# Kernel tuning notes

Hardware: AMD Instinct MI355X
Metric: run time of the kernel (lower is better)

The kernel has to match this reference:

```python
import jax, jax.numpy as jnp
import numpy as np

B, H, S, D = 4, 16, 2048, 64


def setup_inputs() -> dict:
    key = jax.random.key(0)
    kq, kk, kv = jax.random.split(key, 3)
    q = jax.random.normal(kq, (B, H, S, D), dtype=jnp.float32)
    k = jax.random.normal(kk, (B, H, S, D), dtype=jnp.float32)
    v = jax.random.normal(kv, (B, H, S, D), dtype=jnp.float32)
    # causal mask: 1 = keep, 0 = masked (matches masked_fill(mask == 0, -10000))
    mask = jnp.tril(jnp.ones((S, S), dtype=jnp.int32))[None, None, :, :]
    return {"q": q, "k": k, "v": v, "mask": mask}


def reference(q, k, v, mask):
    head_dim = q.shape[3]
    # [b,h,s,t] attention logits
    attn = jnp.einsum("bhsd,bhtd->bhst", q, k) / jnp.sqrt(jnp.float32(head_dim))
    attn = jnp.where(mask == 0, jnp.float32(-10000.0), attn)
    score = jax.nn.softmax(attn, axis=-1)
    # dropout is identity at inference (eval mode)
    return jnp.einsum("bhst,bhtd->bhsd", score, v)
```

## Files before the change

kernel.cpp:

```cpp
#include <hip/hip_runtime.h>
#include <hip/hip_bf16.h>

typedef __bf16 bf16_t;
typedef bf16_t bf16x8 __attribute__((ext_vector_type(8)));
typedef float  f32x4  __attribute__((ext_vector_type(4)));
typedef float  f32x16 __attribute__((ext_vector_type(16)));
typedef int    i32x4  __attribute__((ext_vector_type(4)));

#define DH 64

__device__ __forceinline__ unsigned pkbf(float a, float b) {
    union { bf16_t h[2]; unsigned u; } z;
    z.h[0] = (bf16_t)a; z.h[1] = (bf16_t)b;
    return z.u;
}


__global__ __launch_bounds__(256, 2)
void sdpa_fwd(const float* __restrict__ Qg, const float* __restrict__ Kg,
              const float* __restrict__ Vg, float* __restrict__ Og)
{
    __shared__ char lds[2 * 16384];

    const int n  = blockIdx.x;
    const int o  = ((n & 7) << 6) | (n >> 3);
    const int bh = o >> 3;
    const int pr = o & 7;

    const int t   = threadIdx.x;
    const int w   = t >> 6;
    const int l31 = t & 31;
    const int hi  = (t >> 5) & 1;
    const int swk = (l31 & 7) << 4;

    const size_t hoff = (size_t)bh * 2048 * DH;
    const float* Qh = Qg + hoff;
    const float* Kh = Kg + hoff;
    const float* Vh = Vg + hoff;
    float*       Oh = Og + hoff;

    const int srow = (t >> 3) * 2;
    const int sdc  = t & 7;

    f32x4 rk[4], rv[4];
    {
        const float* kp = Kh + (size_t)srow * DH + sdc * 8;
        rk[0] = *(const f32x4*)kp;        rk[1] = *(const f32x4*)(kp + 4);
        rk[2] = *(const f32x4*)(kp + DH); rk[3] = *(const f32x4*)(kp + DH + 4);
        const float* vp = Vh + (size_t)srow * DH + sdc * 8;
        rv[0] = *(const f32x4*)vp;        rv[1] = *(const f32x4*)(vp + 4);
        rv[2] = *(const f32x4*)(vp + DH); rv[3] = *(const f32x4*)(vp + DH + 4);
    }

    const int stripes[2] = { 15 - pr, pr };
    int gt = 0;

    for (int s = 0; s < 2; ++s) {
        const int p    = stripes[s];
        const int qS   = p * 128;
        const int nkt  = 2 * p + 2;
        const int qsb  = qS + w * 32;
        const int qrow = qsb + l31;
        const int ktd  = qsb >> 6;

        bf16x8 qf[4];
#pragma unroll
        for (int sd = 0; sd < 4; ++sd) {
            const float* qp = Qh + (size_t)qrow * DH + sd * 16 + hi * 8;
            f32x4 a = *(const f32x4*)qp;
            f32x4 b = *(const f32x4*)(qp + 4);
            bf16x8 f;
            f[0] = (bf16_t)(a[0]*0.125f); f[1] = (bf16_t)(a[1]*0.125f);
            f[2] = (bf16_t)(a[2]*0.125f); f[3] = (bf16_t)(a[3]*0.125f);
            f[4] = (bf16_t)(b[0]*0.125f); f[5] = (bf16_t)(b[1]*0.125f);
            f[6] = (bf16_t)(b[2]*0.125f); f[7] = (bf16_t)(b[3]*0.125f);
            qf[sd] = f;
        }

        f32x16 acc0 = {}, acc1 = {};
        float m_run = -1e30f, l_run = 0.0f;

        for (int kt = 0; kt < nkt; ++kt, ++gt) {
            char* kb_ = lds + (gt & 1) * 16384;
            char* vb_ = kb_ + 8192;

            {
#pragma unroll
                for (int r2 = 0; r2 < 2; ++r2) {
                    const int key = srow + r2;
                    bf16x8 f;
                    f[0] = (bf16_t)rk[r2*2][0]; f[1] = (bf16_t)rk[r2*2][1];
                    f[2] = (bf16_t)rk[r2*2][2]; f[3] = (bf16_t)rk[r2*2][3];
                    f[4] = (bf16_t)rk[r2*2+1][0]; f[5] = (bf16_t)rk[r2*2+1][1];
                    f[6] = (bf16_t)rk[r2*2+1][2]; f[7] = (bf16_t)rk[r2*2+1][3];
                    *(bf16x8*)(kb_ + ((key * 128 + sdc * 16) ^ ((key & 7) << 4))) = f;
                }
#pragma unroll
                for (int jj = 0; jj < 8; ++jj) {
                    const int d  = sdc * 8 + jj;
                    const float x0 = (jj < 4) ? rv[0][jj & 3] : rv[1][jj & 3];
                    const float x1 = (jj < 4) ? rv[2][jj & 3] : rv[3][jj & 3];
                    *(unsigned*)(vb_ + ((d * 128 + srow * 2) ^ (((jj ^ sdc) & 7) << 4)))
                        = pkbf(x0, x1);
                }
            }
            if (!(s == 1 && kt == nkt - 1)) {
                const int nk = (kt + 1 < nkt) ? kt + 1 : 0;
                const float* kp = Kh + (size_t)(nk * 64 + srow) * DH + sdc * 8;
                rk[0] = *(const f32x4*)kp;        rk[1] = *(const f32x4*)(kp + 4);
                rk[2] = *(const f32x4*)(kp + DH); rk[3] = *(const f32x4*)(kp + DH + 4);
                const float* vp = Vh + (size_t)(nk * 64 + srow) * DH + sdc * 8;
                rv[0] = *(const f32x4*)vp;        rv[1] = *(const f32x4*)(vp + 4);
                rv[2] = *(const f32x4*)(vp + DH); rv[3] = *(const f32x4*)(vp + DH + 4);
            }
            __syncthreads();

            if (kt * 64 <= qsb + 31) {
                f32x16 tf0 = {}, tf1 = {};
#pragma unroll
                for (int sd = 0; sd < 4; ++sd) {
                    const int inner = sd * 32 + hi * 16;
                    const bf16x8 k0 = *(const bf16x8*)(kb_ + ((l31 * 128 + inner) ^ swk));
                    const bf16x8 k1 = *(const bf16x8*)(kb_ + (((32 + l31) * 128 + inner) ^ swk));
                    tf0 = __builtin_amdgcn_mfma_f32_32x32x16_bf16(k0, qf[sd], tf0, 0, 0, 0);
                    tf1 = __builtin_amdgcn_mfma_f32_32x32x16_bf16(k1, qf[sd], tf1, 0, 0, 0);
                }

                if (kt == ktd) {
#pragma unroll
                    for (int r = 0; r < 16; ++r) {
                        const int krow = kt * 64 + (r & 3) + 8 * (r >> 2) + 4 * hi;
                        if (krow > qrow)      tf0[r] = -10000.0f;
                        if (krow + 32 > qrow) tf1[r] = -10000.0f;
                    }
                }

                float mx = tf0[0];
#pragma unroll
                for (int r = 1; r < 16; ++r) mx = fmaxf(mx, tf0[r]);
#pragma unroll
                for (int r = 0; r < 16; ++r) mx = fmaxf(mx, tf1[r]);
                mx = fmaxf(mx, __shfl_xor(mx, 32));

                if (!__all(mx <= m_run + 8.0f)) {
                    const float mnew  = fmaxf(m_run, mx);
                    const float alpha = __expf(m_run - mnew);
                    m_run = mnew;
                    l_run *= alpha;
                    acc0 *= alpha;
                    acc1 *= alpha;
                }

                float sum = 0.0f;
#pragma unroll
                for (int r = 0; r < 16; ++r) { tf0[r] = __expf(tf0[r] - m_run); sum += tf0[r]; }
#pragma unroll
                for (int r = 0; r < 16; ++r) { tf1[r] = __expf(tf1[r] - m_run); sum += tf1[r]; }
                sum += __shfl_xor(sum, 32);
                l_run += sum;

                unsigned P0[2][4], P1[2][4];
#pragma unroll
                for (int rg = 0; rg < 4; ++rg) {
                    P0[0][rg] = pkbf(tf0[rg * 4 + 0], tf0[rg * 4 + 1]);
                    P1[0][rg] = pkbf(tf0[rg * 4 + 2], tf0[rg * 4 + 3]);
                    P0[1][rg] = pkbf(tf1[rg * 4 + 0], tf1[rg * 4 + 1]);
                    P1[1][rg] = pkbf(tf1[rg * 4 + 2], tf1[rg * 4 + 3]);
                }

#pragma unroll
                for (int sidx = 0; sidx < 4; ++sidx) {
                    const int kb  = sidx >> 1;
                    const int rgl = (sidx & 1) * 2, rgh = rgl + 1;
                    int w0, w1, w2, w3;
#if defined(__has_builtin) && __has_builtin(__builtin_amdgcn_permlane32_swap)
                    auto r0 = __builtin_amdgcn_permlane32_swap((int)P0[kb][rgl], (int)P0[kb][rgh], false, false);
                    auto r1 = __builtin_amdgcn_permlane32_swap((int)P1[kb][rgl], (int)P1[kb][rgh], false, false);
                    w0 = r0[0]; w2 = r0[1]; w1 = r1[0]; w3 = r1[1];
#else
                    const int sa0 = __shfl_xor((int)P0[kb][rgl], 32);
                    const int sb0 = __shfl_xor((int)P0[kb][rgh], 32);
                    const int sa1 = __shfl_xor((int)P1[kb][rgl], 32);
                    const int sb1 = __shfl_xor((int)P1[kb][rgh], 32);
                    w0 = hi ? sb0 : (int)P0[kb][rgl];
                    w2 = hi ? (int)P0[kb][rgh] : sa0;
                    w1 = hi ? sb1 : (int)P1[kb][rgl];
                    w3 = hi ? (int)P1[kb][rgh] : sa1;
#endif
                    union { i32x4 i; bf16x8 v; } pz;
                    pz.i = (i32x4){ w0, w1, w2, w3 };

                    const int inner = sidx * 32 + hi * 16;
                    const int d0 = l31;
                    const int d1 = 32 + l31;
                    const int sz0 = (((d0 & 7) ^ (d0 >> 3)) & 7) << 4;
                    const int sz1 = (((d1 & 7) ^ (d1 >> 3)) & 7) << 4;
                    const bf16x8 v0 = *(const bf16x8*)(vb_ + ((d0 * 128 + inner) ^ sz0));
                    const bf16x8 v1 = *(const bf16x8*)(vb_ + ((d1 * 128 + inner) ^ sz1));
                    acc0 = __builtin_amdgcn_mfma_f32_32x32x16_bf16(v0, pz.v, acc0, 0, 0, 0);
                    acc1 = __builtin_amdgcn_mfma_f32_32x32x16_bf16(v1, pz.v, acc1, 0, 0, 0);
                }
            }
        }

        const float inv = 1.0f / l_run;
        float* op = Oh + (size_t)qrow * DH;
#pragma unroll
        for (int rq = 0; rq < 4; ++rq) {
            f32x4 o0, o1;
#pragma unroll
            for (int j = 0; j < 4; ++j) {
                o0[j] = acc0[rq * 4 + j] * inv;
                o1[j] = acc1[rq * 4 + j] * inv;
            }
            *(f32x4*)(op + 8 * rq + 4 * hi)      = o0;
            *(f32x4*)(op + 32 + 8 * rq + 4 * hi) = o1;
        }
    }
}

extern "C" void kernel_launch(void* const* d_in, const int* in_sizes, int n_in,
                              void* d_out, int out_size, void* d_ws, size_t ws_size,
                              hipStream_t stream) {
    (void)in_sizes; (void)n_in; (void)d_ws; (void)ws_size; (void)out_size;
    const float* q = (const float*)d_in[0];
    const float* k = (const float*)d_in[1];
    const float* v = (const float*)d_in[2];
    float* out = (float*)d_out;
    hipLaunchKernelGGL(sdpa_fwd, dim3(512), dim3(256), 0, stream, q, k, v, out);
}
```

Measured before the change: 75.33 us.

## Split KV range across two wave groups per block and merge softmax partials in LDS

Doubles the block to 512 threads. Two groups of four waves each process half of the key tiles for the same query stripe, with separate double-buffered LDS regions, and their running max, sum and accumulators are combined through LDS at the end. It also folds log2(e) into the Q scale so the kernel can use exp2 instead of exp, and adjusts the mask value and rescale threshold to match. The goal is to halve the serial KV loop per stripe and raise the number of waves in flight. The cost is extra LDS traffic and barriers at each merge, plus heavier LDS use per block, which may limit how many blocks fit on a CU.

```diff
diff --git a/kernel.cpp b/kernel.cpp
--- a/kernel.cpp
+++ b/kernel.cpp
@@ -15,23 +15,36 @@
     return z.u;
 }
 
-
-__global__ __launch_bounds__(256, 2)
+#if defined(__has_builtin)
+#  if __has_builtin(__builtin_amdgcn_exp2f)
+#    define EXP2F(x) __builtin_amdgcn_exp2f(x)
+#  else
+#    define EXP2F(x) exp2f(x)
+#  endif
+#else
+#  define EXP2F(x) exp2f(x)
+#endif
+
+
+__global__ __launch_bounds__(512, 4)
 void sdpa_fwd(const float* __restrict__ Qg, const float* __restrict__ Kg,
               const float* __restrict__ Vg, float* __restrict__ Og)
 {
-    __shared__ char lds[2 * 16384];
+    __shared__ char lds[65536];
 
     const int n  = blockIdx.x;
     const int o  = ((n & 7) << 6) | (n >> 3);
     const int bh = o >> 3;
     const int pr = o & 7;
 
-    const int t   = threadIdx.x;
-    const int w   = t >> 6;
-    const int l31 = t & 31;
-    const int hi  = (t >> 5) & 1;
-    const int swk = (l31 & 7) << 4;
+    const int t    = threadIdx.x;
+    const int w    = t >> 6;
+    const int strm = w >> 2;
+    const int w4   = w & 3;
+    const int l63  = t & 63;
+    const int l31  = t & 31;
+    const int hi   = (t >> 5) & 1;
+    const int swk  = (l31 & 7) << 4;
 
     const size_t hoff = (size_t)bh * 2048 * DH;
     const float* Qh = Qg + hoff;
@@ -39,27 +52,32 @@
     const float* Vh = Vg + hoff;
     float*       Oh = Og + hoff;
 
-    const int srow = (t >> 3) * 2;
-    const int sdc  = t & 7;
+    const int st   = t & 255;
+    const int srow = (st >> 3) * 2;
+    const int sdc  = st & 7;
+
+    const int stripes[2] = { 15 - pr, pr };
+    const int iters[2]   = { 16 - pr, pr + 1 };
 
     f32x4 rk[4], rv[4];
     {
-        const float* kp = Kh + (size_t)srow * DH + sdc * 8;
+        const int kt0 = strm * iters[0];
+        const float* kp = Kh + (size_t)(kt0 * 64 + srow) * DH + sdc * 8;
         rk[0] = *(const f32x4*)kp;        rk[1] = *(const f32x4*)(kp + 4);
         rk[2] = *(const f32x4*)(kp + DH); rk[3] = *(const f32x4*)(kp + DH + 4);
-        const float* vp = Vh + (size_t)srow * DH + sdc * 8;
+        const float* vp = Vh + (size_t)(kt0 * 64 + srow) * DH + sdc * 8;
         rv[0] = *(const f32x4*)vp;        rv[1] = *(const f32x4*)(vp + 4);
         rv[2] = *(const f32x4*)(vp + DH); rv[3] = *(const f32x4*)(vp + DH + 4);
     }
 
-    const int stripes[2] = { 15 - pr, pr };
-    int gt = 0;
-
+    float* cb = (float*)lds;
+    const float QSCALE = 0.125f * 1.44269504088896f;
+
+    int gi = 0;
     for (int s = 0; s < 2; ++s) {
         const int p    = stripes[s];
-        const int qS   = p * 128;
-        const int nkt  = 2 * p + 2;
-        const int qsb  = qS + w * 32;
+        const int h    = iters[s];
+        const int qsb  = p * 128 + w4 * 32;
         const int qrow = qsb + l31;
         const int ktd  = qsb >> 6;
 
@@ -70,18 +88,18 @@
             f32x4 a = *(const f32x4*)qp;
             f32x4 b = *(const f32x4*)(qp + 4);
             bf16x8 f;
-            f[0] = (bf16_t)(a[0]*0.125f); f[1] = (bf16_t)(a[1]*0.125f);
-            f[2] = (bf16_t)(a[2]*0.125f); f[3] = (bf16_t)(a[3]*0.125f);
-            f[4] = (bf16_t)(b[0]*0.125f); f[5] = (bf16_t)(b[1]*0.125f);
-            f[6] = (bf16_t)(b[2]*0.125f); f[7] = (bf16_t)(b[3]*0.125f);
+            f[0] = (bf16_t)(a[0]*QSCALE); f[1] = (bf16_t)(a[1]*QSCALE);
+            f[2] = (bf16_t)(a[2]*QSCALE); f[3] = (bf16_t)(a[3]*QSCALE);
+            f[4] = (bf16_t)(b[0]*QSCALE); f[5] = (bf16_t)(b[1]*QSCALE);
+            f[6] = (bf16_t)(b[2]*QSCALE); f[7] = (bf16_t)(b[3]*QSCALE);
             qf[sd] = f;
         }
 
         f32x16 acc0 = {}, acc1 = {};
         float m_run = -1e30f, l_run = 0.0f;
 
-        for (int kt = 0; kt < nkt; ++kt, ++gt) {
-            char* kb_ = lds + (gt & 1) * 16384;
+        for (int i = 0; i < h; ++i, ++gi) {
+            char* kb_ = lds + strm * 32768 + (gi & 1) * 16384;
             char* vb_ = kb_ + 8192;
 
             {
@@ -89,8 +107,8 @@
                 for (int r2 = 0; r2 < 2; ++r2) {
                     const int key = srow + r2;
                     bf16x8 f;
-                    f[0] = (bf16_t)rk[r2*2][0]; f[1] = (bf16_t)rk[r2*2][1];
-                    f[2] = (bf16_t)rk[r2*2][2]; f[3] = (bf16_t)rk[r2*2][3];
+                    f[0] = (bf16_t)rk[r2*2][0];   f[1] = (bf16_t)rk[r2*2][1];
+                    f[2] = (bf16_t)rk[r2*2][2];   f[3] = (bf16_t)rk[r2*2][3];
                     f[4] = (bf16_t)rk[r2*2+1][0]; f[5] = (bf16_t)rk[r2*2+1][1];
                     f[6] = (bf16_t)rk[r2*2+1][2]; f[7] = (bf16_t)rk[r2*2+1][3];
                     *(bf16x8*)(kb_ + ((key * 128 + sdc * 16) ^ ((key & 7) << 4))) = f;
@@ -104,18 +122,23 @@
                         = pkbf(x0, x1);
                 }
             }
-            if (!(s == 1 && kt == nkt - 1)) {
-                const int nk = (kt + 1 < nkt) ? kt + 1 : 0;
-                const float* kp = Kh + (size_t)(nk * 64 + srow) * DH + sdc * 8;
-                rk[0] = *(const f32x4*)kp;        rk[1] = *(const f32x4*)(kp + 4);
-                rk[2] = *(const f32x4*)(kp + DH); rk[3] = *(const f32x4*)(kp + DH + 4);
-                const float* vp = Vh + (size_t)(nk * 64 + srow) * DH + sdc * 8;
-                rv[0] = *(const f32x4*)vp;        rv[1] = *(const f32x4*)(vp + 4);
-                rv[2] = *(const f32x4*)(vp + DH); rv[3] = *(const f32x4*)(vp + DH + 4);
+            {
+                int ni = i + 1, ns = s;
+                if (ni >= h) { ns = s + 1; ni = 0; }
+                if (ns < 2) {
+                    const int nk = strm * iters[ns] + ni;
+                    const float* kp = Kh + (size_t)(nk * 64 + srow) * DH + sdc * 8;
+                    rk[0] = *(const f32x4*)kp;        rk[1] = *(const f32x4*)(kp + 4);
+                    rk[2] = *(const f32x4*)(kp + DH); rk[3] = *(const f32x4*)(kp + DH + 4);
+                    const float* vp = Vh + (size_t)(nk * 64 + srow) * DH + sdc * 8;
+                    rv[0] = *(const f32x4*)vp;        rv[1] = *(const f32x4*)(vp + 4);
+                    rv[2] = *(const f32x4*)(vp + DH); rv[3] = *(const f32x4*)(vp + DH + 4);
+                }
             }
             __syncthreads();
 
-            if (kt * 64 <= qsb + 31) {
+            const int ktc = strm * h + i;
+            if (ktc <= ktd) {
                 f32x16 tf0 = {}, tf1 = {};
 #pragma unroll
                 for (int sd = 0; sd < 4; ++sd) {
@@ -126,12 +149,12 @@
                     tf1 = __builtin_amdgcn_mfma_f32_32x32x16_bf16(k1, qf[sd], tf1, 0, 0, 0);
                 }
 
-                if (kt == ktd) {
+                if (ktc == ktd) {
 #pragma unroll
                     for (int r = 0; r < 16; ++r) {
-                        const int krow = kt * 64 + (r & 3) + 8 * (r >> 2) + 4 * hi;
-                        if (krow > qrow)      tf0[r] = -10000.0f;
-                        if (krow + 32 > qrow) tf1[r] = -10000.0f;
+                        const int krow = ktc * 64 + (r & 3) + 8 * (r >> 2) + 4 * hi;
+                        if (krow > qrow)      tf0[r] = -20000.0f;
+                        if (krow + 32 > qrow) tf1[r] = -20000.0f;
                     }
                 }
 
@@ -142,9 +165,9 @@
                 for (int r = 0; r < 16; ++r) mx = fmaxf(mx, tf1[r]);
                 mx = fmaxf(mx, __shfl_xor(mx, 32));
 
-                if (!__all(mx <= m_run + 8.0f)) {
+                if (!__all(mx <= m_run + 11.0f)) {
                     const float mnew  = fmaxf(m_run, mx);
-                    const float alpha = __expf(m_run - mnew);
+                    const float alpha = EXP2F(m_run - mnew);
                     m_run = mnew;
                     l_run *= alpha;
                     acc0 *= alpha;
@@ -153,9 +176,9 @@
 
                 float sum = 0.0f;
 #pragma unroll
-                for (int r = 0; r < 16; ++r) { tf0[r] = __expf(tf0[r] - m_run); sum += tf0[r]; }
-#pragma unroll
-                for (int r = 0; r < 16; ++r) { tf1[r] = __expf(tf1[r] - m_run); sum += tf1[r]; }
+                for (int r = 0; r < 16; ++r) { tf0[r] = EXP2F(tf0[r] - m_run); sum += tf0[r]; }
+#pragma unroll
+                for (int r = 0; r < 16; ++r) { tf1[r] = EXP2F(tf1[r] - m_run); sum += tf1[r]; }
                 sum += __shfl_xor(sum, 32);
                 l_run += sum;
 
@@ -187,8 +210,8 @@
                     w1 = hi ? sb1 : (int)P1[kb][rgl];
                     w3 = hi ? (int)P1[kb][rgh] : sa1;
 #endif
-                    union { i32x4 i; bf16x8 v; } pz;
-                    pz.i = (i32x4){ w0, w1, w2, w3 };
+                    union { i32x4 ii; bf16x8 v; } pz;
+                    pz.ii = (i32x4){ w0, w1, w2, w3 };
 
                     const int inner = sidx * 32 + hi * 16;
                     const int d0 = l31;
@@ -203,19 +226,37 @@
             }
         }
 
-        const float inv = 1.0f / l_run;
-        float* op = Oh + (size_t)qrow * DH;
-#pragma unroll
-        for (int rq = 0; rq < 4; ++rq) {
-            f32x4 o0, o1;
-#pragma unroll
-            for (int j = 0; j < 4; ++j) {
-                o0[j] = acc0[rq * 4 + j] * inv;
-                o1[j] = acc1[rq * 4 + j] * inv;
-            }
-            *(f32x4*)(op + 8 * rq + 4 * hi)      = o0;
-            *(f32x4*)(op + 32 + 8 * rq + 4 * hi) = o1;
-        }
+        __syncthreads();
+        const int cbase = (w4 * 64 + l63) * 35;
+        if (strm == 1) {
+#pragma unroll
+            for (int r = 0; r < 16; ++r) { cb[cbase + r] = acc0[r]; cb[cbase + 16 + r] = acc1[r]; }
+            cb[cbase + 32] = m_run;
+            cb[cbase + 33] = l_run;
+        }
+        __syncthreads();
+        if (strm == 0) {
+            const float m_b = cb[cbase + 32];
+            const float l_b = cb[cbase + 33];
+            const float mst = fmaxf(m_run, m_b);
+            const float aa  = EXP2F(m_run - mst);
+            const float ab  = EXP2F(m_b  - mst);
+            const float inv = 1.0f / (l_run * aa + l_b * ab);
+
+            float* op = Oh + (size_t)qrow * DH;
+#pragma unroll
+            for (int rq = 0; rq < 4; ++rq) {
+                f32x4 o0, o1;
+#pragma unroll
+                for (int j = 0; j < 4; ++j) {
+                    o0[j] = (acc0[rq*4+j] * aa + cb[cbase + rq*4 + j]      * ab) * inv;
+                    o1[j] = (acc1[rq*4+j] * aa + cb[cbase + 16 + rq*4 + j] * ab) * inv;
+                }
+                *(f32x4*)(op + 8 * rq + 4 * hi)      = o0;
+                *(f32x4*)(op + 32 + 8 * rq + 4 * hi) = o1;
+            }
+        }
+        __syncthreads();
     }
 }
 
@@ -227,5 +268,5 @@
     const float* k = (const float*)d_in[1];
     const float* v = (const float*)d_in[2];
     float* out = (float*)d_out;
-    hipLaunchKernelGGL(sdpa_fwd, dim3(512), dim3(256), 0, stream, q, k, v, out);
+    hipLaunchKernelGGL(sdpa_fwd, dim3(512), dim3(512), 0, stream, q, k, v, out);
 }
```

After: 201.2 us. 167% more time.

## Stage next K/V tile during compute, use exp2 with folded log2e, add setprio

Applied to the files above, without the earlier changes.

Reorganizes the K/V pipeline so the next tile is converted and written into the alternate LDS buffer before computing on the current one, with global loads issued two tiles ahead and a single barrier at the end of each iteration. The aim is to hide LDS staging and global-load latency behind the MFMA work. It also folds log2(e) into the Q scale so softmax can use the hardware exp2, adjusting the mask constant and rescale threshold to match, and raises wave priority around the MFMA blocks. The prologue adds an extra staging step, and the deeper prefetch raises register pressure.

```diff
diff --git a/kernel.cpp b/kernel.cpp
--- a/kernel.cpp
+++ b/kernel.cpp
@@ -15,6 +15,16 @@
     return z.u;
 }
 
+#if defined(__has_builtin)
+#  if __has_builtin(__builtin_amdgcn_exp2f)
+#    define EXP2F(x) __builtin_amdgcn_exp2f(x)
+#  else
+#    define EXP2F(x) exp2f(x)
+#  endif
+#else
+#  define EXP2F(x) exp2f(x)
+#endif
+
 
 __global__ __launch_bounds__(256, 2)
 void sdpa_fwd(const float* __restrict__ Qg, const float* __restrict__ Kg,
@@ -42,24 +52,55 @@
     const int srow = (t >> 3) * 2;
     const int sdc  = t & 7;
 
+    const int p0  = 15 - pr;
+    const int nk0 = 2 * p0 + 2;
+    const int NT  = 34;
+
     f32x4 rk[4], rv[4];
-    {
-        const float* kp = Kh + (size_t)srow * DH + sdc * 8;
+
+    auto loadKV = [&](int key0) {
+        const float* kp = Kh + (size_t)(key0 + srow) * DH + sdc * 8;
         rk[0] = *(const f32x4*)kp;        rk[1] = *(const f32x4*)(kp + 4);
         rk[2] = *(const f32x4*)(kp + DH); rk[3] = *(const f32x4*)(kp + DH + 4);
-        const float* vp = Vh + (size_t)srow * DH + sdc * 8;
+        const float* vp = Vh + (size_t)(key0 + srow) * DH + sdc * 8;
         rv[0] = *(const f32x4*)vp;        rv[1] = *(const f32x4*)(vp + 4);
         rv[2] = *(const f32x4*)(vp + DH); rv[3] = *(const f32x4*)(vp + DH + 4);
-    }
-
-    const int stripes[2] = { 15 - pr, pr };
+    };
+    auto stageTo = [&](char* kb_, char* vb_) {
+#pragma unroll
+        for (int r2 = 0; r2 < 2; ++r2) {
+            const int key = srow + r2;
+            bf16x8 f;
+            f[0] = (bf16_t)rk[r2*2][0];   f[1] = (bf16_t)rk[r2*2][1];
+            f[2] = (bf16_t)rk[r2*2][2];   f[3] = (bf16_t)rk[r2*2][3];
+            f[4] = (bf16_t)rk[r2*2+1][0]; f[5] = (bf16_t)rk[r2*2+1][1];
+            f[6] = (bf16_t)rk[r2*2+1][2]; f[7] = (bf16_t)rk[r2*2+1][3];
+            *(bf16x8*)(kb_ + ((key * 128 + sdc * 16) ^ ((key & 7) << 4))) = f;
+        }
+#pragma unroll
+        for (int jj = 0; jj < 8; ++jj) {
+            const int d  = sdc * 8 + jj;
+            const float x0 = (jj < 4) ? rv[0][jj & 3] : rv[1][jj & 3];
+            const float x1 = (jj < 4) ? rv[2][jj & 3] : rv[3][jj & 3];
+            *(unsigned*)(vb_ + ((d * 128 + srow * 2) ^ (((jj ^ sdc) & 7) << 4)))
+                = pkbf(x0, x1);
+        }
+    };
+    auto keybase = [&](int g) { return ((g < nk0) ? g : g - nk0) * 64; };
+
+    const float QSCALE = 0.125f * 1.44269504088896f;
+
+    loadKV(0);
+    stageTo(lds, lds + 8192);
+    loadKV(keybase(1));
+    __syncthreads();
+
     int gt = 0;
-
+    const int stripes[2] = { p0, pr };
     for (int s = 0; s < 2; ++s) {
         const int p    = stripes[s];
-        const int qS   = p * 128;
-        const int nkt  = 2 * p + 2;
-        const int qsb  = qS + w * 32;
+        const int h    = 2 * p + 2;
+        const int qsb  = p * 128 + w * 32;
         const int qrow = qsb + l31;
         const int ktd  = qsb >> 6;
 
@@ -70,53 +111,29 @@
             f32x4 a = *(const f32x4*)qp;
             f32x4 b = *(const f32x4*)(qp + 4);
             bf16x8 f;
-            f[0] = (bf16_t)(a[0]*0.125f); f[1] = (bf16_t)(a[1]*0.125f);
-            f[2] = (bf16_t)(a[2]*0.125f); f[3] = (bf16_t)(a[3]*0.125f);
-            f[4] = (bf16_t)(b[0]*0.125f); f[5] = (bf16_t)(b[1]*0.125f);
-            f[6] = (bf16_t)(b[2]*0.125f); f[7] = (bf16_t)(b[3]*0.125f);
+            f[0] = (bf16_t)(a[0]*QSCALE); f[1] = (bf16_t)(a[1]*QSCALE);
+            f[2] = (bf16_t)(a[2]*QSCALE); f[3] = (bf16_t)(a[3]*QSCALE);
+            f[4] = (bf16_t)(b[0]*QSCALE); f[5] = (bf16_t)(b[1]*QSCALE);
+            f[6] = (bf16_t)(b[2]*QSCALE); f[7] = (bf16_t)(b[3]*QSCALE);
             qf[sd] = f;
         }
 
         f32x16 acc0 = {}, acc1 = {};
         float m_run = -1e30f, l_run = 0.0f;
 
-        for (int kt = 0; kt < nkt; ++kt, ++gt) {
-            char* kb_ = lds + (gt & 1) * 16384;
-            char* vb_ = kb_ + 8192;
-
-            {
-#pragma unroll
-                for (int r2 = 0; r2 < 2; ++r2) {
-                    const int key = srow + r2;
-                    bf16x8 f;
-                    f[0] = (bf16_t)rk[r2*2][0]; f[1] = (bf16_t)rk[r2*2][1];
-                    f[2] = (bf16_t)rk[r2*2][2]; f[3] = (bf16_t)rk[r2*2][3];
-                    f[4] = (bf16_t)rk[r2*2+1][0]; f[5] = (bf16_t)rk[r2*2+1][1];
-                    f[6] = (bf16_t)rk[r2*2+1][2]; f[7] = (bf16_t)rk[r2*2+1][3];
-                    *(bf16x8*)(kb_ + ((key * 128 + sdc * 16) ^ ((key & 7) << 4))) = f;
-                }
-#pragma unroll
-                for (int jj = 0; jj < 8; ++jj) {
-                    const int d  = sdc * 8 + jj;
-                    const float x0 = (jj < 4) ? rv[0][jj & 3] : rv[1][jj & 3];
-                    const float x1 = (jj < 4) ? rv[2][jj & 3] : rv[3][jj & 3];
-                    *(unsigned*)(vb_ + ((d * 128 + srow * 2) ^ (((jj ^ sdc) & 7) << 4)))
-                        = pkbf(x0, x1);
-                }
-            }
-            if (!(s == 1 && kt == nkt - 1)) {
-                const int nk = (kt + 1 < nkt) ? kt + 1 : 0;
-                const float* kp = Kh + (size_t)(nk * 64 + srow) * DH + sdc * 8;
-                rk[0] = *(const f32x4*)kp;        rk[1] = *(const f32x4*)(kp + 4);
-                rk[2] = *(const f32x4*)(kp + DH); rk[3] = *(const f32x4*)(kp + DH + 4);
-                const float* vp = Vh + (size_t)(nk * 64 + srow) * DH + sdc * 8;
-                rv[0] = *(const f32x4*)vp;        rv[1] = *(const f32x4*)(vp + 4);
-                rv[2] = *(const f32x4*)(vp + DH); rv[3] = *(const f32x4*)(vp + DH + 4);
-            }
-            __syncthreads();
-
-            if (kt * 64 <= qsb + 31) {
+        for (int i = 0; i < h; ++i, ++gt) {
+            char* cb_ = lds + (gt & 1) * 16384;
+            char* sb_ = lds + ((gt + 1) & 1) * 16384;
+
+            if (gt + 1 < NT) stageTo(sb_, sb_ + 8192);
+            if (gt + 2 < NT) loadKV(keybase(gt + 2));
+
+            if (i <= ktd) {
+                char* kb_ = cb_;
+                char* vb_ = cb_ + 8192;
+
                 f32x16 tf0 = {}, tf1 = {};
+                __builtin_amdgcn_s_setprio(1);
 #pragma unroll
                 for (int sd = 0; sd < 4; ++sd) {
                     const int inner = sd * 32 + hi * 16;
@@ -125,13 +142,14 @@
                     tf0 = __builtin_amdgcn_mfma_f32_32x32x16_bf16(k0, qf[sd], tf0, 0, 0, 0);
                     tf1 = __builtin_amdgcn_mfma_f32_32x32x16_bf16(k1, qf[sd], tf1, 0, 0, 0);
                 }
-
-                if (kt == ktd) {
+                __builtin_amdgcn_s_setprio(0);
+
+                if (i == ktd) {
 #pragma unroll
                     for (int r = 0; r < 16; ++r) {
-                        const int krow = kt * 64 + (r & 3) + 8 * (r >> 2) + 4 * hi;
-                        if (krow > qrow)      tf0[r] = -10000.0f;
-                        if (krow + 32 > qrow) tf1[r] = -10000.0f;
+                        const int krow = i * 64 + (r & 3) + 8 * (r >> 2) + 4 * hi;
+                        if (krow > qrow)      tf0[r] = -20000.0f;
+                        if (krow + 32 > qrow) tf1[r] = -20000.0f;
                     }
                 }
 
@@ -142,9 +160,9 @@
                 for (int r = 0; r < 16; ++r) mx = fmaxf(mx, tf1[r]);
                 mx = fmaxf(mx, __shfl_xor(mx, 32));
 
-                if (!__all(mx <= m_run + 8.0f)) {
+                if (!__all(mx <= m_run + 11.0f)) {
                     const float mnew  = fmaxf(m_run, mx);
-                    const float alpha = __expf(m_run - mnew);
+                    const float alpha = EXP2F(m_run - mnew);
                     m_run = mnew;
                     l_run *= alpha;
                     acc0 *= alpha;
@@ -153,9 +171,9 @@
 
                 float sum = 0.0f;
 #pragma unroll
-                for (int r = 0; r < 16; ++r) { tf0[r] = __expf(tf0[r] - m_run); sum += tf0[r]; }
-#pragma unroll
-                for (int r = 0; r < 16; ++r) { tf1[r] = __expf(tf1[r] - m_run); sum += tf1[r]; }
+                for (int r = 0; r < 16; ++r) { tf0[r] = EXP2F(tf0[r] - m_run); sum += tf0[r]; }
+#pragma unroll
+                for (int r = 0; r < 16; ++r) { tf1[r] = EXP2F(tf1[r] - m_run); sum += tf1[r]; }
                 sum += __shfl_xor(sum, 32);
                 l_run += sum;
 
@@ -168,6 +186,7 @@
                     P1[1][rg] = pkbf(tf1[rg * 4 + 2], tf1[rg * 4 + 3]);
                 }
 
+                __builtin_amdgcn_s_setprio(1);
 #pragma unroll
                 for (int sidx = 0; sidx < 4; ++sidx) {
                     const int kb  = sidx >> 1;
@@ -187,8 +206,8 @@
                     w1 = hi ? sb1 : (int)P1[kb][rgl];
                     w3 = hi ? (int)P1[kb][rgh] : sa1;
 #endif
-                    union { i32x4 i; bf16x8 v; } pz;
-                    pz.i = (i32x4){ w0, w1, w2, w3 };
+                    union { i32x4 ii; bf16x8 v; } pz;
+                    pz.ii = (i32x4){ w0, w1, w2, w3 };
 
                     const int inner = sidx * 32 + hi * 16;
                     const int d0 = l31;
@@ -200,7 +219,9 @@
                     acc0 = __builtin_amdgcn_mfma_f32_32x32x16_bf16(v0, pz.v, acc0, 0, 0, 0);
                     acc1 = __builtin_amdgcn_mfma_f32_32x32x16_bf16(v1, pz.v, acc1, 0, 0, 0);
                 }
+                __builtin_amdgcn_s_setprio(0);
             }
+            __syncthreads();
         }
 
         const float inv = 1.0f / l_run;
```

Result: no change. 73.89 us (-1.9%).
